# Performance work log

Measured on AMD Instinct MI355X. Metric: run time of the kernel, lower is better.

Reference implementation:

```python
import jax, jax.numpy as jnp
import numpy as np

N_LEVELS = 16
N_FEATS = 2
LOG2_T = 19
TABLE_SIZE = 2 ** LOG2_T
BASE_RES = 16
PER_LEVEL_SCALE = 1.3819
N_PTS = 524288
# per-level grid resolutions (static)
RESOLUTIONS = np.floor(BASE_RES * PER_LEVEL_SCALE ** np.arange(N_LEVELS)).astype(np.float32)
# NGP spatial hash primes for 2D
PRIME0 = np.uint32(1)
PRIME1 = np.uint32(2654435761)
# corner offsets for bilinear interp: (0,0),(0,1),(1,0),(1,1)
CORNER_OFFS = np.array([[0, 0], [0, 1], [1, 0], [1, 1]], dtype=np.uint32)


def setup_inputs() -> dict:
    key = jax.random.key(0)
    k1, k2 = jax.random.split(key)
    pts = jax.random.uniform(k1, (N_PTS, 3), dtype=jnp.float32)  # coords in [0,1]
    # 3 planes x L levels x T entries x F features, small init like NGP (1e-4)
    tables = jax.random.normal(k2, (3, N_LEVELS, TABLE_SIZE, N_FEATS), dtype=jnp.float32) * 1e-4
    return {"pts": pts, "tables": tables}


def _encode_plane(coords, table):
    # coords: [N,2] in [0,1]; table: [L,T,F]
    L, T, F = table.shape
    res = jnp.asarray(RESOLUTIONS)  # [L]
    scaled = coords[None, :, :] * res[:, None, None]  # [L,N,2]
    x0 = jnp.floor(scaled)
    frac = scaled - x0  # [L,N,2]
    x0u = x0.astype(jnp.uint32)
    offs = jnp.asarray(CORNER_OFFS)  # [4,2]
    corners = x0u[:, :, None, :] + offs[None, None, :, :]  # [L,N,4,2]
    # NGP spatial hash with uint32 wraparound, then mod table size
    h = (corners[..., 0] * PRIME0) ^ (corners[..., 1] * PRIME1)  # [L,N,4] uint32
    idx = (h % jnp.uint32(T)).astype(jnp.int32)  # [L,N,4]
    feats = table[jnp.arange(L)[:, None, None], idx]  # [L,N,4,F]
    # bilinear weights: product over dims of frac (offset=1) or 1-frac (offset=0)
    fo = offs.astype(coords.dtype)  # [4,2]
    w = jnp.prod(jnp.where(fo[None, None] > 0, frac[:, :, None, :], 1.0 - frac[:, :, None, :]), axis=-1)  # [L,N,4]
    out = jnp.einsum('lnc,lncf->lnf', w, feats)  # [L,N,F]
    return out.transpose(1, 0, 2).reshape(coords.shape[0], L * F)  # [N, L*F]


def reference(pts, tables):
    # coordinate-pair planes: combinations of (0,1,2) taken 2 at a time
    coo_combs = [(0, 1), (0, 2), (1, 2)]
    interp_space = 1.0
    for ci, comb in enumerate(coo_combs):
        interp_space = interp_space * _encode_plane(pts[:, list(comb)], tables[ci])
    return interp_space  # [N, 32]
```

## Files before the change

kernel.cpp:

```cpp
#include <hip/hip_runtime.h>
#include <stdint.h>


#define NPTS   524288u
#define TSIZE  524288u
#define TMASK  0x7FFFFu
#define PRIME1 2654435761u

__constant__ float c_res[16] = {
    16.f, 22.f, 30.f, 42.f, 58.f, 80.f, 111.f, 153.f,
    212.f, 294.f, 406.f, 561.f, 775.f, 1072.f, 1481.f, 2047.f
};
__constant__ int c_resiLow[12] = {16, 22, 30, 42, 58, 80, 111, 153, 212, 294, 406, 561};

__global__ __launch_bounds__(256) void k_packhist(
    const float* __restrict__ pts, float2* __restrict__ pts2,
    uint32_t* __restrict__ hist)
{
    __shared__ uint32_t lh[768];
    const uint32_t b = blockIdx.x, t = threadIdx.x;
    lh[t] = 0u; lh[t + 256u] = 0u; lh[t + 512u] = 0u;
    __syncthreads();
    const uint32_t pt = b * 256u + t;
    const float x = pts[pt * 3u + 0u];
    const float y = pts[pt * 3u + 1u];
    const float z = pts[pt * 3u + 2u];
    pts2[            pt] = make_float2(x, y);
    pts2[NPTS      + pt] = make_float2(x, z);
    pts2[2u * NPTS + pt] = make_float2(y, z);
    const uint32_t bx = min(15u, (uint32_t)(x * 16.f));
    const uint32_t by = min(15u, (uint32_t)(y * 16.f));
    const uint32_t bz = min(15u, (uint32_t)(z * 16.f));
    atomicAdd(&lh[         bx * 16u + by], 1u);
    atomicAdd(&lh[256u +   bx * 16u + bz], 1u);
    atomicAdd(&lh[512u +   by * 16u + bz], 1u);
    __syncthreads();
    if (lh[t])        atomicAdd(&hist[t],        lh[t]);
    if (lh[t + 256u]) atomicAdd(&hist[t + 256u], lh[t + 256u]);
    if (lh[t + 512u]) atomicAdd(&hist[t + 512u], lh[t + 512u]);
}

__global__ __launch_bounds__(256) void k_scatter(
    const float2* __restrict__ pts2, const uint32_t* __restrict__ hist,
    uint32_t* __restrict__ cursor, float4* __restrict__ sort16)
{
    __shared__ uint32_t su[256], lcnt[256], gb[256], lc2[256];
    const uint32_t b = blockIdx.x, t = threadIdx.x;
    const uint32_t plane = b >> 6, chunk = b & 63u;
    const uint32_t h = hist[plane * 256u + t];
    su[t] = h; lcnt[t] = 0u; lc2[t] = 0u;
    __syncthreads();
    for (uint32_t off = 1u; off < 256u; off <<= 1) {
        uint32_t v = 0u;
        if (t >= off) v = su[t - off];
        __syncthreads();
        su[t] += v;
        __syncthreads();
    }
    const uint32_t mybase = su[t] - h;
    const float2* __restrict__ pp = pts2 + (size_t)plane * NPTS;
    const uint32_t pt0 = chunk * 8192u + t;
    for (uint32_t k = 0; k < 32u; ++k) {
        const float2 c = pp[pt0 + k * 256u];
        const uint32_t bb = min(15u, (uint32_t)(c.x * 16.f)) * 16u
                          + min(15u, (uint32_t)(c.y * 16.f));
        atomicAdd(&lcnt[bb], 1u);
    }
    __syncthreads();
    gb[t] = mybase + atomicAdd(&cursor[plane * 256u + t], lcnt[t]);
    __syncthreads();
    float4* __restrict__ sp = sort16 + (size_t)plane * NPTS;
    for (uint32_t k = 0; k < 32u; ++k) {
        const uint32_t pt = pt0 + k * 256u;
        const float2 c = pp[pt];
        const uint32_t bb = min(15u, (uint32_t)(c.x * 16.f)) * 16u
                          + min(15u, (uint32_t)(c.y * 16.f));
        const uint32_t r = atomicAdd(&lc2[bb], 1u);
        sp[gb[bb] + r] = make_float4(c.x, c.y, __uint_as_float(pt), 0.f);
    }
}

__global__ __launch_bounds__(256) void k_lowhi(
    const float2* __restrict__ pts2, const float4* __restrict__ sort16,
    const uint32_t* __restrict__ hist, const float2* __restrict__ tab,
    float2* __restrict__ ws2, float2* __restrict__ wsH)
{
    __shared__ float2 sm[4000];
    const uint32_t b = blockIdx.x, t = threadIdx.x;

    if (b < 768u) {
        const uint32_t plane  = b >> 8;
        const uint32_t bucket = b & 255u;
        const uint32_t bx = bucket >> 4, by = bucket & 15u;

        uint32_t* su = (uint32_t*)sm;
        const uint32_t h = hist[plane * 256u + t];
        su[t] = h;
        __syncthreads();
        for (uint32_t off = 1u; off < 256u; off <<= 1) {
            uint32_t v = 0u;
            if (t >= off) v = su[t - off];
            __syncthreads();
            su[t] += v;
            __syncthreads();
        }
        const uint32_t cntB  = hist[plane * 256u + bucket];
        const uint32_t start = su[bucket] - cntB;
        __syncthreads();

        uint32_t* Pm = (uint32_t*)(sm + 3968);
        if (t == 0u) {
            uint32_t off = 0u;
            for (uint32_t l = 0; l < 12u; ++l) {
                const int R = c_resiLow[l];
                const int u0s = max(0, (int)((bx * (uint32_t)R) >> 4) - 1);
                const int u0e = min(R, (int)(((bx + 1u) * (uint32_t)R) >> 4) + 2);
                const int u1s = max(0, (int)((by * (uint32_t)R) >> 4) - 1);
                const int u1e = min(R, (int)(((by + 1u) * (uint32_t)R) >> 4) + 2);
                const uint32_t rows = (uint32_t)(u0e - u0s + 1);
                const uint32_t cols = (uint32_t)(u1e - u1s + 1);
                Pm[l] = off; Pm[12u + l] = (uint32_t)u0s;
                Pm[24u + l] = (uint32_t)u1s; Pm[36u + l] = cols;
                Pm[48u + l] = rows;
                off += rows * cols;
            }
        }
        __syncthreads();

        for (uint32_t l = 0; l < 12u; ++l) {
            const uint32_t off  = Pm[l];
            const uint32_t u0s  = Pm[12u + l], u1s = Pm[24u + l];
            const uint32_t cols = Pm[36u + l], rows = Pm[48u + l];
            const uint32_t E    = rows * cols;
            const uint32_t tb   = (plane * 16u + l) * TSIZE;
            for (uint32_t i = t; i < E; i += 256u) {
                const uint32_t r  = i / cols;
                const uint32_t cx = u0s + r;
                const uint32_t cy = u1s + (i - r * cols);
                sm[off + i] = tab[tb + ((cx ^ (cy * PRIME1)) & TMASK)];
            }
        }
        __syncthreads();

        const float4* __restrict__ sp = sort16 + (size_t)plane * NPTS;
        float4* __restrict__ w4 = (float4*)ws2;
        for (uint32_t i = t; i < cntB; i += 256u) {
            const float4 f = sp[start + i];
            const float c0 = f.x, c1 = f.y;
            const uint32_t orig = __float_as_uint(f.z);
            float2 acc[12];
#pragma unroll
            for (int l = 0; l < 12; ++l) {
                const float res = c_res[l];
                const float s0 = c0 * res;
                const float s1 = c1 * res;
                const float f0 = floorf(s0);
                const float f1 = floorf(s1);
                const float r0 = s0 - f0;
                const float r1 = s1 - f1;
                const uint32_t u0 = (uint32_t)f0, u1 = (uint32_t)f1;
                const uint32_t cols = Pm[36u + l];
                const uint32_t ci = Pm[l] + (u0 - Pm[12u + l]) * cols
                                  + (u1 - Pm[24u + l]);
                const float2 q00 = sm[ci];
                const float2 q01 = sm[ci + 1u];
                const float2 q10 = sm[ci + cols];
                const float2 q11 = sm[ci + cols + 1u];
                const float w00 = (1.f - r0) * (1.f - r1);
                const float w01 = (1.f - r0) * r1;
                const float w10 = r0 * (1.f - r1);
                const float w11 = r0 * r1;
                acc[l] = make_float2(
                    w00 * q00.x + w01 * q01.x + w10 * q10.x + w11 * q11.x,
                    w00 * q00.y + w01 * q01.y + w10 * q10.y + w11 * q11.y);
            }
            const size_t d = (size_t)orig * 18u + (size_t)plane * 6u;
            w4[d + 0] = make_float4(acc[0].x, acc[0].y, acc[1].x, acc[1].y);
            w4[d + 1] = make_float4(acc[2].x, acc[2].y, acc[3].x, acc[3].y);
            w4[d + 2] = make_float4(acc[4].x, acc[4].y, acc[5].x, acc[5].y);
            w4[d + 3] = make_float4(acc[6].x, acc[6].y, acc[7].x, acc[7].y);
            w4[d + 4] = make_float4(acc[8].x, acc[8].y, acc[9].x, acc[9].y);
            w4[d + 5] = make_float4(acc[10].x, acc[10].y, acc[11].x, acc[11].y);
        }
        return;
    }

    const uint32_t hb  = b - 768u;
    const uint32_t xcd = hb & 7u;
    const uint32_t s   = hb >> 3;
    uint32_t g, chunk;
    if (s < 512u) { g = xcd; chunk = s; }
    else { g = 8u + (xcd >> 1); chunk = ((xcd & 1u) << 8) + (s - 512u); }
    const uint32_t plane = g % 3u;
    const uint32_t lvl   = 12u + g / 3u;
    const uint32_t gabs  = plane * 16u + lvl;
    const float    res   = c_res[lvl];
    const uint32_t tb    = gabs * TSIZE;
    const float4* __restrict__ tab4 = (const float4*)tab;
    const uint32_t b4    = gabs * (TSIZE / 2u);
    const float2* __restrict__ pp = pts2 + (size_t)plane * NPTS;
    const uint32_t pt0   = chunk * 1024u + t;

    float4 P0[4], P1[4];
    float2 Q0[4], Q1[4];
    float  r0[4], r1[4];
    uint32_t sel0[4], sel1[4], oddm[4];

#pragma unroll
    for (int k = 0; k < 4; ++k) {
        const uint32_t pt = pt0 + (uint32_t)k * 256u;
        const float2 c2 = pp[pt];
        const float s0 = c2.x * res;
        const float s1 = c2.y * res;
        const float f0 = floorf(s0);
        const float f1 = floorf(s1);
        r0[k] = s0 - f0;
        r1[k] = s1 - f1;
        const uint32_t u0  = (uint32_t)f0;
        const uint32_t hy0 = (uint32_t)f1 * PRIME1;
        const uint32_t hy1 = hy0 + PRIME1;
        const uint32_t i00 = ( u0        ^ hy0) & TMASK;
        const uint32_t i01 = ( u0        ^ hy1) & TMASK;
        const uint32_t i10 = ((u0 + 1u)  ^ hy0) & TMASK;
        const uint32_t i11 = ((u0 + 1u)  ^ hy1) & TMASK;
        sel0[k] = i00 & 1u;
        sel1[k] = i01 & 1u;
        oddm[k] = u0 & 1u;
        P0[k] = tab4[b4 + (i00 >> 1)];
        P1[k] = tab4[b4 + (i01 >> 1)];
        Q0[k] = make_float2(0.f, 0.f);
        Q1[k] = make_float2(0.f, 0.f);
        if (oddm[k]) {
            Q0[k] = tab[tb + i10];
            Q1[k] = tab[tb + i11];
        }
    }
#pragma unroll
    for (int k = 0; k < 4; ++k) {
        const uint32_t pt = pt0 + (uint32_t)k * 256u;
        const float2 lo0 = make_float2(P0[k].x, P0[k].y);
        const float2 hi0 = make_float2(P0[k].z, P0[k].w);
        const float2 lo1 = make_float2(P1[k].x, P1[k].y);
        const float2 hi1 = make_float2(P1[k].z, P1[k].w);
        const float2 t00 = sel0[k] ? hi0 : lo0;
        const float2 t01 = sel1[k] ? hi1 : lo1;
        const float2 t10 = oddm[k] ? Q0[k] : (sel0[k] ? lo0 : hi0);
        const float2 t11 = oddm[k] ? Q1[k] : (sel1[k] ? lo1 : hi1);
        const float w00 = (1.f - r0[k]) * (1.f - r1[k]);
        const float w01 = (1.f - r0[k]) * r1[k];
        const float w10 = r0[k] * (1.f - r1[k]);
        const float w11 = r0[k] * r1[k];
        wsH[(size_t)g * NPTS + pt] = make_float2(
            w00 * t00.x + w01 * t01.x + w10 * t10.x + w11 * t11.x,
            w00 * t00.y + w01 * t01.y + w10 * t10.y + w11 * t11.y);
    }
}

__global__ __launch_bounds__(256) void k_comb(
    const float2* __restrict__ ws2, const float2* __restrict__ wsH,
    float2* __restrict__ out)
{
    __shared__ float2 s2[2304];
    __shared__ float2 sh[768];
    const uint32_t b = blockIdx.x, t = threadIdx.x;
    const uint32_t pt0 = b * 64u;
    const float2* __restrict__ src = ws2 + (size_t)pt0 * 36u;
    for (uint32_t i = t; i < 2304u; i += 256u) s2[i] = src[i];
    for (uint32_t i = t; i < 768u; i += 256u) {
        const uint32_t j = i >> 6, p = i & 63u;
        sh[i] = wsH[(size_t)j * NPTS + pt0 + p];
    }
    __syncthreads();
#pragma unroll
    for (uint32_t k = 0; k < 4u; ++k) {
        const uint32_t e = t + k * 256u;
        const uint32_t pt = e >> 4, l = e & 15u;
        float2 v;
        if (l < 12u) {
            const float2 a  = s2[pt * 36u + l];
            const float2 bb = s2[pt * 36u + 12u + l];
            const float2 c  = s2[pt * 36u + 24u + l];
            v = make_float2(a.x * bb.x * c.x, a.y * bb.y * c.y);
        } else {
            const uint32_t j0 = (l - 12u) * 3u;
            const float2 a  = sh[j0 * 64u + pt];
            const float2 bb = sh[(j0 + 1u) * 64u + pt];
            const float2 c  = sh[(j0 + 2u) * 64u + pt];
            v = make_float2(a.x * bb.x * c.x, a.y * bb.y * c.y);
        }
        out[(size_t)(pt0 + pt) * 16u + l] = v;
    }
}

template <int P, bool FIRST>
__global__ __launch_bounds__(256) void kplane_pass(
    const float* __restrict__ pts, const float2* __restrict__ tab,
    float2* __restrict__ ws)
{
    const uint32_t b     = blockIdx.x;
    const uint32_t xcd   = b & 7u;
    const uint32_t s     = b >> 3;
    const uint32_t gi    = s >> 11;
    const uint32_t chunk = s & 2047u;
    const uint32_t lvl   = gi * 8u + xcd;
    const uint32_t pt    = chunk * 256u + threadIdx.x;
    constexpr int c0 = (P == 2) ? 1 : 0;
    constexpr int c1 = (P == 0) ? 1 : 2;
    const float a0  = pts[pt * 3u + c0];
    const float a1  = pts[pt * 3u + c1];
    const float res = c_res[lvl];
    const float s0 = a0 * res;
    const float s1 = a1 * res;
    const float f0 = floorf(s0);
    const float f1 = floorf(s1);
    const float r0 = s0 - f0;
    const float r1 = s1 - f1;
    const uint32_t u0 = (uint32_t)f0;
    const uint32_t hy0  = (uint32_t)f1 * PRIME1;
    const uint32_t hy1  = hy0 + PRIME1;
    const uint32_t base = ((uint32_t)P * 16u + lvl) * TSIZE;
    const float2 t00 = tab[base + (( u0       ^ hy0) & TMASK)];
    const float2 t01 = tab[base + (( u0       ^ hy1) & TMASK)];
    const float2 t10 = tab[base + (((u0 + 1u) ^ hy0) & TMASK)];
    const float2 t11 = tab[base + (((u0 + 1u) ^ hy1) & TMASK)];
    const float w00 = (1.f - r0) * (1.f - r1);
    const float w01 = (1.f - r0) * r1;
    const float w10 = r0 * (1.f - r1);
    const float w11 = r0 * r1;
    const float e0 = w00 * t00.x + w01 * t01.x + w10 * t10.x + w11 * t11.x;
    const float e1 = w00 * t00.y + w01 * t01.y + w10 * t10.y + w11 * t11.y;
    const uint32_t widx = lvl * NPTS + pt;
    if (FIRST) {
        ws[widx] = make_float2(e0, e1);
    } else {
        const float2 prev = ws[widx];
        ws[widx] = make_float2(prev.x * e0, prev.y * e1);
    }
}

__global__ __launch_bounds__(256) void kplane_transpose(
    const float2* __restrict__ ws, float2* __restrict__ out)
{
    const uint32_t tid = blockIdx.x * 256u + threadIdx.x;
    const uint32_t lvl = tid & 15u;
    const uint32_t pt  = tid >> 4;
    out[tid] = ws[lvl * NPTS + pt];
}

__global__ __launch_bounds__(256) void kplane_mono(
    const float* __restrict__ pts, const float2* __restrict__ tab,
    float2* __restrict__ out)
{
    const uint32_t tid = blockIdx.x * 256u + threadIdx.x;
    const uint32_t pt  = tid >> 4;
    const uint32_t lvl = tid & 15u;
    const float x = pts[pt * 3u + 0u];
    const float y = pts[pt * 3u + 1u];
    const float z = pts[pt * 3u + 2u];
    const float res = c_res[lvl];
    const float a0[3] = {x, x, y};
    const float a1[3] = {y, z, z};
    float p0 = 1.f, p1 = 1.f;
#pragma unroll
    for (int pl = 0; pl < 3; ++pl) {
        const float s0 = a0[pl] * res;
        const float s1 = a1[pl] * res;
        const float f0 = floorf(s0);
        const float f1 = floorf(s1);
        const float r0 = s0 - f0;
        const float r1 = s1 - f1;
        const uint32_t u0 = (uint32_t)f0;
        const uint32_t hy0 = (uint32_t)f1 * PRIME1;
        const uint32_t hy1 = hy0 + PRIME1;
        const uint32_t base = ((uint32_t)pl * 16u + lvl) * TSIZE;
        const float2 t00 = tab[base + (( u0       ^ hy0) & TMASK)];
        const float2 t01 = tab[base + (( u0       ^ hy1) & TMASK)];
        const float2 t10 = tab[base + (((u0 + 1u) ^ hy0) & TMASK)];
        const float2 t11 = tab[base + (((u0 + 1u) ^ hy1) & TMASK)];
        const float w00 = (1.f - r0) * (1.f - r1);
        const float w01 = (1.f - r0) * r1;
        const float w10 = r0 * (1.f - r1);
        const float w11 = r0 * r1;
        p0 *= w00 * t00.x + w01 * t01.x + w10 * t10.x + w11 * t11.x;
        p1 *= w00 * t00.y + w01 * t01.y + w10 * t10.y + w11 * t11.y;
    }
    out[pt * 16u + lvl] = make_float2(p0, p1);
}

extern "C" void kernel_launch(void* const* d_in, const int* in_sizes, int n_in,
                              void* d_out, int out_size, void* d_ws, size_t ws_size,
                              hipStream_t stream) {
    const float*  pts = (const float*)d_in[0];
    const float2* tab = (const float2*)d_in[1];
    float2*       out = (float2*)d_out;

    const size_t wsA = (size_t)48 * NPTS * sizeof(float2);
    const size_t wsB = (size_t)16 * NPTS * sizeof(float2);
    dim3 block256(256u);

    if (ws_size >= wsA) {
        float2*   pts2   = (float2*)d_out;
        float4*   sort16 = (float4*)(pts2 + (size_t)3 * NPTS);
        uint32_t* hist   = (uint32_t*)(sort16 + (size_t)3 * NPTS);
        uint32_t* cursor = hist + 768;
        float2* ws2 = (float2*)d_ws;
        float2* wsH = ws2 + (size_t)36 * NPTS;

        hipMemsetAsync(hist, 0, 1536u * sizeof(uint32_t), stream);
        hipLaunchKernelGGL(k_packhist, dim3(2048u), block256, 0, stream,
                           pts, pts2, hist);
        hipLaunchKernelGGL(k_scatter,  dim3(192u),  block256, 0, stream,
                           pts2, hist, cursor, sort16);
        hipLaunchKernelGGL(k_lowhi,    dim3(6912u), block256, 0, stream,
                           pts2, sort16, hist, tab, ws2, wsH);
        hipLaunchKernelGGL(k_comb,     dim3(NPTS / 64u), block256, 0, stream,
                           ws2, wsH, out);
    } else if (ws_size >= wsB) {
        float2* ws = (float2*)d_ws;
        dim3 grid(16u * (NPTS / 256u));
        hipLaunchKernelGGL((kplane_pass<0, true >), grid, block256, 0, stream, pts, tab, ws);
        hipLaunchKernelGGL((kplane_pass<1, false>), grid, block256, 0, stream, pts, tab, ws);
        hipLaunchKernelGGL((kplane_pass<2, false>), grid, block256, 0, stream, pts, tab, ws);
        dim3 tgrid((NPTS * 16u) / 256u);
        hipLaunchKernelGGL(kplane_transpose, tgrid, block256, 0, stream, ws, out);
    } else {
        dim3 grid((NPTS * 16u) / 256u);
        hipLaunchKernelGGL(kplane_mono, grid, block256, 0, stream, pts, tab, out);
    }
}
```

Before: 282.1 us.

## Split low levels into dense shared-memory passes and fuse plane products for high levels

Levels 0-5 are now handled by unsorted streaming blocks that load each full small grid (or a half of level 5) into shared memory. Only levels 6-11 keep the bucket-sorted tiled path, which shrinks the per-bucket tile. The high levels 12-15 now compute all three planes per thread and write the product directly, removing the per-plane intermediate writes. The packed points are stored once as float4 instead of three float2 planes. Together these cut workspace traffic and per-bucket staging, at the cost of more blocks, branch divergence in the split level-5 pass, and redundant point reads.

```diff
diff --git a/kernel.cpp b/kernel.cpp
--- a/kernel.cpp
+++ b/kernel.cpp
@@ -11,10 +11,12 @@
     16.f, 22.f, 30.f, 42.f, 58.f, 80.f, 111.f, 153.f,
     212.f, 294.f, 406.f, 561.f, 775.f, 1072.f, 1481.f, 2047.f
 };
-__constant__ int c_resiLow[12] = {16, 22, 30, 42, 58, 80, 111, 153, 212, 294, 406, 561};
+__constant__ int      c_resi6[6] = {111, 153, 212, 294, 406, 561};
+__constant__ uint32_t c_R03[4]   = {17, 23, 31, 43};
+__constant__ uint32_t c_off03[4] = {0, 289, 818, 1779};
 
 __global__ __launch_bounds__(256) void k_packhist(
-    const float* __restrict__ pts, float2* __restrict__ pts2,
+    const float* __restrict__ pts, float4* __restrict__ pts4,
     uint32_t* __restrict__ hist)
 {
     __shared__ uint32_t lh[768];
@@ -25,9 +27,7 @@
     const float x = pts[pt * 3u + 0u];
     const float y = pts[pt * 3u + 1u];
     const float z = pts[pt * 3u + 2u];
-    pts2[            pt] = make_float2(x, y);
-    pts2[NPTS      + pt] = make_float2(x, z);
-    pts2[2u * NPTS + pt] = make_float2(y, z);
+    pts4[pt] = make_float4(x, y, z, 0.f);
     const uint32_t bx = min(15u, (uint32_t)(x * 16.f));
     const uint32_t by = min(15u, (uint32_t)(y * 16.f));
     const uint32_t bz = min(15u, (uint32_t)(z * 16.f));
@@ -41,7 +41,7 @@
 }
 
 __global__ __launch_bounds__(256) void k_scatter(
-    const float2* __restrict__ pts2, const uint32_t* __restrict__ hist,
+    const float4* __restrict__ pts4, const uint32_t* __restrict__ hist,
     uint32_t* __restrict__ cursor, float4* __restrict__ sort16)
 {
     __shared__ uint32_t su[256], lcnt[256], gb[256], lc2[256];
@@ -58,12 +58,13 @@
         __syncthreads();
     }
     const uint32_t mybase = su[t] - h;
-    const float2* __restrict__ pp = pts2 + (size_t)plane * NPTS;
     const uint32_t pt0 = chunk * 8192u + t;
     for (uint32_t k = 0; k < 32u; ++k) {
-        const float2 c = pp[pt0 + k * 256u];
-        const uint32_t bb = min(15u, (uint32_t)(c.x * 16.f)) * 16u
-                          + min(15u, (uint32_t)(c.y * 16.f));
+        const float4 c = pts4[pt0 + k * 256u];
+        const float c0 = (plane == 2u) ? c.y : c.x;
+        const float c1 = (plane == 0u) ? c.y : c.z;
+        const uint32_t bb = min(15u, (uint32_t)(c0 * 16.f)) * 16u
+                          + min(15u, (uint32_t)(c1 * 16.f));
         atomicAdd(&lcnt[bb], 1u);
     }
     __syncthreads();
@@ -72,20 +73,25 @@
     float4* __restrict__ sp = sort16 + (size_t)plane * NPTS;
     for (uint32_t k = 0; k < 32u; ++k) {
         const uint32_t pt = pt0 + k * 256u;
-        const float2 c = pp[pt];
-        const uint32_t bb = min(15u, (uint32_t)(c.x * 16.f)) * 16u
-                          + min(15u, (uint32_t)(c.y * 16.f));
+        const float4 c = pts4[pt];
+        const float c0 = (plane == 2u) ? c.y : c.x;
+        const float c1 = (plane == 0u) ? c.y : c.z;
+        const uint32_t bb = min(15u, (uint32_t)(c0 * 16.f)) * 16u
+                          + min(15u, (uint32_t)(c1 * 16.f));
         const uint32_t r = atomicAdd(&lc2[bb], 1u);
-        sp[gb[bb] + r] = make_float4(c.x, c.y, __uint_as_float(pt), 0.f);
-    }
-}
-
-__global__ __launch_bounds__(256) void k_lowhi(
-    const float2* __restrict__ pts2, const float4* __restrict__ sort16,
+        sp[gb[bb] + r] = make_float4(c0, c1, __uint_as_float(pt), 0.f);
+    }
+}
+
+__global__ __launch_bounds__(256) void k_mega(
+    const float4* __restrict__ pts4, const float4* __restrict__ sort16,
     const uint32_t* __restrict__ hist, const float2* __restrict__ tab,
-    float2* __restrict__ ws2, float2* __restrict__ wsH)
-{
-    __shared__ float2 sm[4000];
+    float2* __restrict__ ws05,
+    float2* __restrict__ ws2,
+    float2* __restrict__ wsP)
+{
+    __shared__ float2 sm[3700];
+    __shared__ uint32_t Poff[6], Pu0[6], Pu1[6], Pcols[6], Prows[6];
     const uint32_t b = blockIdx.x, t = threadIdx.x;
 
     if (b < 768u) {
@@ -108,31 +114,28 @@
         const uint32_t start = su[bucket] - cntB;
         __syncthreads();
 
-        uint32_t* Pm = (uint32_t*)(sm + 3968);
         if (t == 0u) {
             uint32_t off = 0u;
-            for (uint32_t l = 0; l < 12u; ++l) {
-                const int R = c_resiLow[l];
+            for (uint32_t l = 0; l < 6u; ++l) {
+                const int R = c_resi6[l];
                 const int u0s = max(0, (int)((bx * (uint32_t)R) >> 4) - 1);
                 const int u0e = min(R, (int)(((bx + 1u) * (uint32_t)R) >> 4) + 2);
                 const int u1s = max(0, (int)((by * (uint32_t)R) >> 4) - 1);
                 const int u1e = min(R, (int)(((by + 1u) * (uint32_t)R) >> 4) + 2);
                 const uint32_t rows = (uint32_t)(u0e - u0s + 1);
                 const uint32_t cols = (uint32_t)(u1e - u1s + 1);
-                Pm[l] = off; Pm[12u + l] = (uint32_t)u0s;
-                Pm[24u + l] = (uint32_t)u1s; Pm[36u + l] = cols;
-                Pm[48u + l] = rows;
+                Poff[l] = off; Pu0[l] = (uint32_t)u0s; Pu1[l] = (uint32_t)u1s;
+                Pcols[l] = cols; Prows[l] = rows;
                 off += rows * cols;
             }
         }
         __syncthreads();
 
-        for (uint32_t l = 0; l < 12u; ++l) {
-            const uint32_t off  = Pm[l];
-            const uint32_t u0s  = Pm[12u + l], u1s = Pm[24u + l];
-            const uint32_t cols = Pm[36u + l], rows = Pm[48u + l];
-            const uint32_t E    = rows * cols;
-            const uint32_t tb   = (plane * 16u + l) * TSIZE;
+        for (uint32_t l = 0; l < 6u; ++l) {
+            const uint32_t off = Poff[l], u0s = Pu0[l], u1s = Pu1[l];
+            const uint32_t cols = Pcols[l];
+            const uint32_t E = Prows[l] * cols;
+            const uint32_t tb = (plane * 16u + 6u + l) * TSIZE;
             for (uint32_t i = t; i < E; i += 256u) {
                 const uint32_t r  = i / cols;
                 const uint32_t cx = u0s + r;
@@ -148,10 +151,10 @@
             const float4 f = sp[start + i];
             const float c0 = f.x, c1 = f.y;
             const uint32_t orig = __float_as_uint(f.z);
-            float2 acc[12];
-#pragma unroll
-            for (int l = 0; l < 12; ++l) {
-                const float res = c_res[l];
+            float2 acc[6];
+#pragma unroll
+            for (int l = 0; l < 6; ++l) {
+                const float res = c_res[6 + l];
                 const float s0 = c0 * res;
                 const float s1 = c1 * res;
                 const float f0 = floorf(s0);
@@ -159,9 +162,8 @@
                 const float r0 = s0 - f0;
                 const float r1 = s1 - f1;
                 const uint32_t u0 = (uint32_t)f0, u1 = (uint32_t)f1;
-                const uint32_t cols = Pm[36u + l];
-                const uint32_t ci = Pm[l] + (u0 - Pm[12u + l]) * cols
-                                  + (u1 - Pm[24u + l]);
+                const uint32_t cols = Pcols[l];
+                const uint32_t ci = Poff[l] + (u0 - Pu0[l]) * cols + (u1 - Pu1[l]);
                 const float2 q00 = sm[ci];
                 const float2 q01 = sm[ci + 1u];
                 const float2 q10 = sm[ci + cols];
@@ -174,48 +176,165 @@
                     w00 * q00.x + w01 * q01.x + w10 * q10.x + w11 * q11.x,
                     w00 * q00.y + w01 * q01.y + w10 * q10.y + w11 * q11.y);
             }
-            const size_t d = (size_t)orig * 18u + (size_t)plane * 6u;
+            const size_t d = (size_t)orig * 9u + (size_t)plane * 3u;
             w4[d + 0] = make_float4(acc[0].x, acc[0].y, acc[1].x, acc[1].y);
             w4[d + 1] = make_float4(acc[2].x, acc[2].y, acc[3].x, acc[3].y);
             w4[d + 2] = make_float4(acc[4].x, acc[4].y, acc[5].x, acc[5].y);
-            w4[d + 3] = make_float4(acc[6].x, acc[6].y, acc[7].x, acc[7].y);
-            w4[d + 4] = make_float4(acc[8].x, acc[8].y, acc[9].x, acc[9].y);
-            w4[d + 5] = make_float4(acc[10].x, acc[10].y, acc[11].x, acc[11].y);
         }
         return;
     }
 
-    const uint32_t hb  = b - 768u;
+    if (b < 1152u) {
+        const uint32_t bb    = b - 768u;
+        const uint32_t set   = bb >> 5;
+        const uint32_t chunk = bb & 31u;
+        const uint32_t plane = set >> 2;
+        const uint32_t kind  = set & 3u;
+        const uint32_t pt0   = chunk * 16384u + t;
+
+        if (kind == 0u) {
+#pragma unroll
+            for (int l = 0; l < 4; ++l) {
+                const uint32_t R = c_R03[l], off = c_off03[l], E = R * R;
+                const uint32_t tb = (plane * 16u + (uint32_t)l) * TSIZE;
+                for (uint32_t i = t; i < E; i += 256u) {
+                    const uint32_t cx = i / R, cy = i - cx * R;
+                    sm[off + i] = tab[tb + ((cx ^ (cy * PRIME1)) & TMASK)];
+                }
+            }
+            __syncthreads();
+            for (uint32_t k = 0; k < 64u; ++k) {
+                const uint32_t pt = pt0 + k * 256u;
+                const float4 c4 = pts4[pt];
+                const float c0 = (plane == 2u) ? c4.y : c4.x;
+                const float c1 = (plane == 0u) ? c4.y : c4.z;
+#pragma unroll
+                for (int l = 0; l < 4; ++l) {
+                    const uint32_t R = c_R03[l], off = c_off03[l];
+                    const float res = c_res[l];
+                    const float s0 = c0 * res;
+                    const float s1 = c1 * res;
+                    const float f0 = floorf(s0);
+                    const float f1 = floorf(s1);
+                    const float r0 = s0 - f0;
+                    const float r1 = s1 - f1;
+                    const uint32_t ci = off + (uint32_t)f0 * R + (uint32_t)f1;
+                    const float2 q00 = sm[ci];
+                    const float2 q01 = sm[ci + 1u];
+                    const float2 q10 = sm[ci + R];
+                    const float2 q11 = sm[ci + R + 1u];
+                    const float w00 = (1.f - r0) * (1.f - r1);
+                    const float w01 = (1.f - r0) * r1;
+                    const float w10 = r0 * (1.f - r1);
+                    const float w11 = r0 * r1;
+                    ws05[(size_t)(plane * 6u + (uint32_t)l) * NPTS + pt] =
+                        make_float2(
+                        w00 * q00.x + w01 * q01.x + w10 * q10.x + w11 * q11.x,
+                        w00 * q00.y + w01 * q01.y + w10 * q10.y + w11 * q11.y);
+                }
+            }
+        } else if (kind == 1u) {
+            const uint32_t R = 59u, E = 3481u;
+            const uint32_t tb = (plane * 16u + 4u) * TSIZE;
+            for (uint32_t i = t; i < E; i += 256u) {
+                const uint32_t cx = i / R, cy = i - cx * R;
+                sm[i] = tab[tb + ((cx ^ (cy * PRIME1)) & TMASK)];
+            }
+            __syncthreads();
+            for (uint32_t k = 0; k < 64u; ++k) {
+                const uint32_t pt = pt0 + k * 256u;
+                const float4 c4 = pts4[pt];
+                const float c0 = (plane == 2u) ? c4.y : c4.x;
+                const float c1 = (plane == 0u) ? c4.y : c4.z;
+                const float s0 = c0 * 58.f;
+                const float s1 = c1 * 58.f;
+                const float f0 = floorf(s0);
+                const float f1 = floorf(s1);
+                const float r0 = s0 - f0;
+                const float r1 = s1 - f1;
+                const uint32_t ci = (uint32_t)f0 * R + (uint32_t)f1;
+                const float2 q00 = sm[ci];
+                const float2 q01 = sm[ci + 1u];
+                const float2 q10 = sm[ci + R];
+                const float2 q11 = sm[ci + R + 1u];
+                const float w00 = (1.f - r0) * (1.f - r1);
+                const float w01 = (1.f - r0) * r1;
+                const float w10 = r0 * (1.f - r1);
+                const float w11 = r0 * r1;
+                ws05[(size_t)(plane * 6u + 4u) * NPTS + pt] = make_float2(
+                    w00 * q00.x + w01 * q01.x + w10 * q10.x + w11 * q11.x,
+                    w00 * q00.y + w01 * q01.y + w10 * q10.y + w11 * q11.y);
+            }
+        } else {
+            const uint32_t lo  = (kind == 2u) ? 0u : 40u;
+            const uint32_t hiX = lo + 40u;
+            const uint32_t R = 81u, E = 41u * 81u;
+            const uint32_t tb = (plane * 16u + 5u) * TSIZE;
+            for (uint32_t i = t; i < E; i += 256u) {
+                const uint32_t r = i / R;
+                const uint32_t cx = lo + r, cy = i - r * R;
+                sm[i] = tab[tb + ((cx ^ (cy * PRIME1)) & TMASK)];
+            }
+            __syncthreads();
+            for (uint32_t k = 0; k < 64u; ++k) {
+                const uint32_t pt = pt0 + k * 256u;
+                const float4 c4 = pts4[pt];
+                const float c0 = (plane == 2u) ? c4.y : c4.x;
+                const float c1 = (plane == 0u) ? c4.y : c4.z;
+                const float s0 = c0 * 80.f;
+                const float s1 = c1 * 80.f;
+                const float f0 = floorf(s0);
+                const float f1 = floorf(s1);
+                const uint32_t u0 = (uint32_t)f0;
+                if (u0 >= lo && u0 < hiX) {
+                    const float r0 = s0 - f0;
+                    const float r1 = s1 - f1;
+                    const uint32_t ci = (u0 - lo) * R + (uint32_t)f1;
+                    const float2 q00 = sm[ci];
+                    const float2 q01 = sm[ci + 1u];
+                    const float2 q10 = sm[ci + R];
+                    const float2 q11 = sm[ci + R + 1u];
+                    const float w00 = (1.f - r0) * (1.f - r1);
+                    const float w01 = (1.f - r0) * r1;
+                    const float w10 = r0 * (1.f - r1);
+                    const float w11 = r0 * r1;
+                    ws05[(size_t)(plane * 6u + 5u) * NPTS + pt] = make_float2(
+                        w00 * q00.x + w01 * q01.x + w10 * q10.x + w11 * q11.x,
+                        w00 * q00.y + w01 * q01.y + w10 * q10.y + w11 * q11.y);
+                }
+            }
+        }
+        return;
+    }
+
+    const uint32_t hb  = b - 1152u;
     const uint32_t xcd = hb & 7u;
     const uint32_t s   = hb >> 3;
-    uint32_t g, chunk;
-    if (s < 512u) { g = xcd; chunk = s; }
-    else { g = 8u + (xcd >> 1); chunk = ((xcd & 1u) << 8) + (s - 512u); }
-    const uint32_t plane = g % 3u;
-    const uint32_t lvl   = 12u + g / 3u;
-    const uint32_t gabs  = plane * 16u + lvl;
-    const float    res   = c_res[lvl];
-    const uint32_t tb    = gabs * TSIZE;
+    const uint32_t lvl = 12u + (xcd >> 1);
+    const uint32_t chunk = ((xcd & 1u) << 10) + s;
+    const uint32_t pt  = chunk * 256u + t;
+    const float4 c4 = pts4[pt];
+    const float pc0[3] = {c4.x, c4.x, c4.y};
+    const float pc1[3] = {c4.y, c4.z, c4.z};
+    const float res = c_res[lvl];
     const float4* __restrict__ tab4 = (const float4*)tab;
-    const uint32_t b4    = gabs * (TSIZE / 2u);
-    const float2* __restrict__ pp = pts2 + (size_t)plane * NPTS;
-    const uint32_t pt0   = chunk * 1024u + t;
-
-    float4 P0[4], P1[4];
-    float2 Q0[4], Q1[4];
-    float  r0[4], r1[4];
-    uint32_t sel0[4], sel1[4], oddm[4];
-
-#pragma unroll
-    for (int k = 0; k < 4; ++k) {
-        const uint32_t pt = pt0 + (uint32_t)k * 256u;
-        const float2 c2 = pp[pt];
-        const float s0 = c2.x * res;
-        const float s1 = c2.y * res;
+
+    float4 P0[3], P1[3];
+    float2 Q0[3], Q1[3];
+    float  r0[3], r1[3];
+    uint32_t sel0[3], sel1[3], oddm[3];
+
+#pragma unroll
+    for (int p = 0; p < 3; ++p) {
+        const uint32_t gabs = (uint32_t)p * 16u + lvl;
+        const uint32_t tb = gabs * TSIZE;
+        const uint32_t b4 = gabs * (TSIZE / 2u);
+        const float s0 = pc0[p] * res;
+        const float s1 = pc1[p] * res;
         const float f0 = floorf(s0);
         const float f1 = floorf(s1);
-        r0[k] = s0 - f0;
-        r1[k] = s1 - f1;
+        r0[p] = s0 - f0;
+        r1[p] = s1 - f1;
         const uint32_t u0  = (uint32_t)f0;
         const uint32_t hy0 = (uint32_t)f1 * PRIME1;
         const uint32_t hy1 = hy0 + PRIME1;
@@ -223,52 +342,57 @@
         const uint32_t i01 = ( u0        ^ hy1) & TMASK;
         const uint32_t i10 = ((u0 + 1u)  ^ hy0) & TMASK;
         const uint32_t i11 = ((u0 + 1u)  ^ hy1) & TMASK;
-        sel0[k] = i00 & 1u;
-        sel1[k] = i01 & 1u;
-        oddm[k] = u0 & 1u;
-        P0[k] = tab4[b4 + (i00 >> 1)];
-        P1[k] = tab4[b4 + (i01 >> 1)];
-        Q0[k] = make_float2(0.f, 0.f);
-        Q1[k] = make_float2(0.f, 0.f);
-        if (oddm[k]) {
-            Q0[k] = tab[tb + i10];
-            Q1[k] = tab[tb + i11];
-        }
-    }
-#pragma unroll
-    for (int k = 0; k < 4; ++k) {
-        const uint32_t pt = pt0 + (uint32_t)k * 256u;
-        const float2 lo0 = make_float2(P0[k].x, P0[k].y);
-        const float2 hi0 = make_float2(P0[k].z, P0[k].w);
-        const float2 lo1 = make_float2(P1[k].x, P1[k].y);
-        const float2 hi1 = make_float2(P1[k].z, P1[k].w);
-        const float2 t00 = sel0[k] ? hi0 : lo0;
-        const float2 t01 = sel1[k] ? hi1 : lo1;
-        const float2 t10 = oddm[k] ? Q0[k] : (sel0[k] ? lo0 : hi0);
-        const float2 t11 = oddm[k] ? Q1[k] : (sel1[k] ? lo1 : hi1);
-        const float w00 = (1.f - r0[k]) * (1.f - r1[k]);
-        const float w01 = (1.f - r0[k]) * r1[k];
-        const float w10 = r0[k] * (1.f - r1[k]);
-        const float w11 = r0[k] * r1[k];
-        wsH[(size_t)g * NPTS + pt] = make_float2(
-            w00 * t00.x + w01 * t01.x + w10 * t10.x + w11 * t11.x,
-            w00 * t00.y + w01 * t01.y + w10 * t10.y + w11 * t11.y);
-    }
+        sel0[p] = i00 & 1u;
+        sel1[p] = i01 & 1u;
+        oddm[p] = u0 & 1u;
+        P0[p] = tab4[b4 + (i00 >> 1)];
+        P1[p] = tab4[b4 + (i01 >> 1)];
+        Q0[p] = make_float2(0.f, 0.f);
+        Q1[p] = make_float2(0.f, 0.f);
+        if (oddm[p]) {
+            Q0[p] = tab[tb + i10];
+            Q1[p] = tab[tb + i11];
+        }
+    }
+    float prod0 = 1.f, prod1 = 1.f;
+#pragma unroll
+    for (int p = 0; p < 3; ++p) {
+        const float2 lo0 = make_float2(P0[p].x, P0[p].y);
+        const float2 hi0 = make_float2(P0[p].z, P0[p].w);
+        const float2 lo1 = make_float2(P1[p].x, P1[p].y);
+        const float2 hi1 = make_float2(P1[p].z, P1[p].w);
+        const float2 t00 = sel0[p] ? hi0 : lo0;
+        const float2 t01 = sel1[p] ? hi1 : lo1;
+        const float2 t10 = oddm[p] ? Q0[p] : (sel0[p] ? lo0 : hi0);
+        const float2 t11 = oddm[p] ? Q1[p] : (sel1[p] ? lo1 : hi1);
+        const float w00 = (1.f - r0[p]) * (1.f - r1[p]);
+        const float w01 = (1.f - r0[p]) * r1[p];
+        const float w10 = r0[p] * (1.f - r1[p]);
+        const float w11 = r0[p] * r1[p];
+        prod0 *= w00 * t00.x + w01 * t01.x + w10 * t10.x + w11 * t11.x;
+        prod1 *= w00 * t00.y + w01 * t01.y + w10 * t10.y + w11 * t11.y;
+    }
+    wsP[(size_t)(lvl - 12u) * NPTS + pt] = make_float2(prod0, prod1);
 }
 
 __global__ __launch_bounds__(256) void k_comb(
-    const float2* __restrict__ ws2, const float2* __restrict__ wsH,
-    float2* __restrict__ out)
-{
-    __shared__ float2 s2[2304];
-    __shared__ float2 sh[768];
+    const float2* __restrict__ ws05, const float2* __restrict__ ws2,
+    const float2* __restrict__ wsP, float2* __restrict__ out)
+{
+    __shared__ float2 s05[1152];
+    __shared__ float2 s2[1152];
+    __shared__ float2 spd[256];
     const uint32_t b = blockIdx.x, t = threadIdx.x;
     const uint32_t pt0 = b * 64u;
-    const float2* __restrict__ src = ws2 + (size_t)pt0 * 36u;
-    for (uint32_t i = t; i < 2304u; i += 256u) s2[i] = src[i];
-    for (uint32_t i = t; i < 768u; i += 256u) {
-        const uint32_t j = i >> 6, p = i & 63u;
-        sh[i] = wsH[(size_t)j * NPTS + pt0 + p];
+    for (uint32_t i = t; i < 1152u; i += 256u) {
+        const uint32_t row = i >> 6, p = i & 63u;
+        s05[i] = ws05[(size_t)row * NPTS + pt0 + p];
+    }
+    const float2* __restrict__ w2src = ws2 + (size_t)pt0 * 18u;
+    for (uint32_t i = t; i < 1152u; i += 256u) s2[i] = w2src[i];
+    {
+        const uint32_t row = t >> 6, p = t & 63u;
+        spd[t] = wsP[(size_t)row * NPTS + pt0 + p];
     }
     __syncthreads();
 #pragma unroll
@@ -276,17 +400,19 @@
         const uint32_t e = t + k * 256u;
         const uint32_t pt = e >> 4, l = e & 15u;
         float2 v;
-        if (l < 12u) {
-            const float2 a  = s2[pt * 36u + l];
-            const float2 bb = s2[pt * 36u + 12u + l];
-            const float2 c  = s2[pt * 36u + 24u + l];
+        if (l < 6u) {
+            const float2 a  = s05[l * 64u + pt];
+            const float2 bb = s05[(6u + l) * 64u + pt];
+            const float2 c  = s05[(12u + l) * 64u + pt];
+            v = make_float2(a.x * bb.x * c.x, a.y * bb.y * c.y);
+        } else if (l < 12u) {
+            const uint32_t j = l - 6u;
+            const float2 a  = s2[pt * 18u + j];
+            const float2 bb = s2[pt * 18u + 6u + j];
+            const float2 c  = s2[pt * 18u + 12u + j];
             v = make_float2(a.x * bb.x * c.x, a.y * bb.y * c.y);
         } else {
-            const uint32_t j0 = (l - 12u) * 3u;
-            const float2 a  = sh[j0 * 64u + pt];
-            const float2 bb = sh[(j0 + 1u) * 64u + pt];
-            const float2 c  = sh[(j0 + 2u) * 64u + pt];
-            v = make_float2(a.x * bb.x * c.x, a.y * bb.y * c.y);
+            v = spd[(l - 12u) * 64u + pt];
         }
         out[(size_t)(pt0 + pt) * 16u + l] = v;
     }
@@ -394,27 +520,28 @@
     const float2* tab = (const float2*)d_in[1];
     float2*       out = (float2*)d_out;
 
-    const size_t wsA = (size_t)48 * NPTS * sizeof(float2);
+    const size_t wsA = (size_t)40 * NPTS * sizeof(float2);
     const size_t wsB = (size_t)16 * NPTS * sizeof(float2);
     dim3 block256(256u);
 
     if (ws_size >= wsA) {
-        float2*   pts2   = (float2*)d_out;
-        float4*   sort16 = (float4*)(pts2 + (size_t)3 * NPTS);
+        float4*   pts4   = (float4*)d_out;
+        float4*   sort16 = pts4 + NPTS;
         uint32_t* hist   = (uint32_t*)(sort16 + (size_t)3 * NPTS);
         uint32_t* cursor = hist + 768;
-        float2* ws2 = (float2*)d_ws;
-        float2* wsH = ws2 + (size_t)36 * NPTS;
+        float2* ws05 = (float2*)d_ws;
+        float2* ws2  = ws05 + (size_t)18 * NPTS;
+        float2* wsP  = ws2  + (size_t)18 * NPTS;
 
         hipMemsetAsync(hist, 0, 1536u * sizeof(uint32_t), stream);
         hipLaunchKernelGGL(k_packhist, dim3(2048u), block256, 0, stream,
-                           pts, pts2, hist);
+                           pts, pts4, hist);
         hipLaunchKernelGGL(k_scatter,  dim3(192u),  block256, 0, stream,
-                           pts2, hist, cursor, sort16);
-        hipLaunchKernelGGL(k_lowhi,    dim3(6912u), block256, 0, stream,
-                           pts2, sort16, hist, tab, ws2, wsH);
+                           pts4, hist, cursor, sort16);
+        hipLaunchKernelGGL(k_mega,     dim3(9344u), block256, 0, stream,
+                           pts4, sort16, hist, tab, ws05, ws2, wsP);
         hipLaunchKernelGGL(k_comb,     dim3(NPTS / 64u), block256, 0, stream,
-                           ws2, wsH, out);
+                           ws05, ws2, wsP, out);
     } else if (ws_size >= wsB) {
         float2* ws = (float2*)d_ws;
         dim3 grid(16u * (NPTS / 256u));
```

Result: slower. 339.1 us (+20.2%).

## Pre-expand low-level hash grids densely, store intermediates as fp16, split low/hi kernels

Applied to the files above, without the earlier changes.

Adds a dense pre-expansion of the 12 low-resolution levels into a contiguous grid inside the pack kernel, so the low-level kernel loads coalesced dense rows instead of scattered hashed gathers. Per-plane intermediate features are now packed as half2 instead of float2, halving workspace write and read traffic in the combine step. The fused low/hi kernel is split into two separate launches. Storing intermediates in fp16 reduces precision before the three-plane product, and the dense buffer adds a layout dependency inside the output region.

```diff
diff --git a/kernel.cpp b/kernel.cpp
--- a/kernel.cpp
+++ b/kernel.cpp
@@ -1,4 +1,5 @@
 #include <hip/hip_runtime.h>
+#include <hip/hip_fp16.h>
 #include <stdint.h>
 
 
@@ -6,19 +7,52 @@
 #define TSIZE  524288u
 #define TMASK  0x7FFFFu
 #define PRIME1 2654435761u
+#define PLANE_D     663817u
+#define DENSE_TOTAL 1991451u
 
 __constant__ float c_res[16] = {
     16.f, 22.f, 30.f, 42.f, 58.f, 80.f, 111.f, 153.f,
     212.f, 294.f, 406.f, 561.f, 775.f, 1072.f, 1481.f, 2047.f
 };
-__constant__ int c_resiLow[12] = {16, 22, 30, 42, 58, 80, 111, 153, 212, 294, 406, 561};
-
-__global__ __launch_bounds__(256) void k_packhist(
-    const float* __restrict__ pts, float2* __restrict__ pts2,
-    uint32_t* __restrict__ hist)
+__constant__ int      c_resiLow[12] = {16, 22, 30, 42, 58, 80, 111, 153, 212, 294, 406, 561};
+__constant__ uint32_t c_RD[12]   = {17, 23, 31, 43, 59, 81, 112, 154, 213, 295, 407, 562};
+__constant__ uint32_t c_offD[12] = {0, 289, 818, 1779, 3628, 7109, 13670,
+                                    26214, 49930, 95299, 182324, 347973};
+
+__device__ __forceinline__ uint32_t pkh2(float a, float b) {
+    __half2 h2;
+    h2.x = __float2half_rn(a);
+    h2.y = __float2half_rn(b);
+    return *reinterpret_cast<const uint32_t*>(&h2);
+}
+__device__ __forceinline__ float2 uph2(uint32_t u) {
+    __half2 h2 = *reinterpret_cast<const __half2*>(&u);
+    return make_float2(__half2float(h2.x), __half2float(h2.y));
+}
+
+__global__ __launch_bounds__(256) void k_packexp(
+    const float* __restrict__ pts, const float2* __restrict__ tab,
+    float2* __restrict__ pts2, uint32_t* __restrict__ hist,
+    float2* __restrict__ dense)
 {
     __shared__ uint32_t lh[768];
     const uint32_t b = blockIdx.x, t = threadIdx.x;
+
+    if (b >= 2048u) {
+        const uint32_t idx = (b - 2048u) * 256u + t;
+        if (idx >= DENSE_TOTAL) return;
+        const uint32_t plane = idx / PLANE_D;
+        const uint32_t i     = idx - plane * PLANE_D;
+        uint32_t lvl = 11u;
+        while (i < c_offD[lvl]) lvl--;
+        const uint32_t RD    = c_RD[lvl];
+        const uint32_t local = i - c_offD[lvl];
+        const uint32_t cx = local / RD, cy = local - cx * RD;
+        dense[idx] =
+            tab[(plane * 16u + lvl) * TSIZE + ((cx ^ (cy * PRIME1)) & TMASK)];
+        return;
+    }
+
     lh[t] = 0u; lh[t + 256u] = 0u; lh[t + 512u] = 0u;
     __syncthreads();
     const uint32_t pt = b * 256u + t;
@@ -80,114 +114,109 @@
     }
 }
 
-__global__ __launch_bounds__(256) void k_lowhi(
-    const float2* __restrict__ pts2, const float4* __restrict__ sort16,
-    const uint32_t* __restrict__ hist, const float2* __restrict__ tab,
-    float2* __restrict__ ws2, float2* __restrict__ wsH)
+__global__ __launch_bounds__(256) void k_low(
+    const float4* __restrict__ sort16, const uint32_t* __restrict__ hist,
+    const float2* __restrict__ dense, uint4* __restrict__ ws2u)
 {
     __shared__ float2 sm[4000];
+    __shared__ uint32_t Poff[12], Pu0[12], Pu1[12], Pcols[12], Prows[12];
     const uint32_t b = blockIdx.x, t = threadIdx.x;
-
-    if (b < 768u) {
-        const uint32_t plane  = b >> 8;
-        const uint32_t bucket = b & 255u;
-        const uint32_t bx = bucket >> 4, by = bucket & 15u;
-
-        uint32_t* su = (uint32_t*)sm;
-        const uint32_t h = hist[plane * 256u + t];
-        su[t] = h;
+    const uint32_t plane  = b >> 8;
+    const uint32_t bucket = b & 255u;
+    const uint32_t bx = bucket >> 4, by = bucket & 15u;
+
+    uint32_t* su = (uint32_t*)sm;
+    const uint32_t h = hist[plane * 256u + t];
+    su[t] = h;
+    __syncthreads();
+    for (uint32_t off = 1u; off < 256u; off <<= 1) {
+        uint32_t v = 0u;
+        if (t >= off) v = su[t - off];
         __syncthreads();
-        for (uint32_t off = 1u; off < 256u; off <<= 1) {
-            uint32_t v = 0u;
-            if (t >= off) v = su[t - off];
-            __syncthreads();
-            su[t] += v;
-            __syncthreads();
+        su[t] += v;
+        __syncthreads();
+    }
+    const uint32_t cntB  = hist[plane * 256u + bucket];
+    const uint32_t start = su[bucket] - cntB;
+    __syncthreads();
+
+    if (t == 0u) {
+        uint32_t off = 0u;
+        for (uint32_t l = 0; l < 12u; ++l) {
+            const int R = c_resiLow[l];
+            const int u0s = max(0, (int)((bx * (uint32_t)R) >> 4) - 1);
+            const int u0e = min(R, (int)(((bx + 1u) * (uint32_t)R) >> 4) + 2);
+            const int u1s = max(0, (int)((by * (uint32_t)R) >> 4) - 1);
+            const int u1e = min(R, (int)(((by + 1u) * (uint32_t)R) >> 4) + 2);
+            const uint32_t rows = (uint32_t)(u0e - u0s + 1);
+            const uint32_t cols = (uint32_t)(u1e - u1s + 1);
+            Poff[l] = off; Pu0[l] = (uint32_t)u0s; Pu1[l] = (uint32_t)u1s;
+            Pcols[l] = cols; Prows[l] = rows;
+            off += rows * cols;
         }
-        const uint32_t cntB  = hist[plane * 256u + bucket];
-        const uint32_t start = su[bucket] - cntB;
-        __syncthreads();
-
-        uint32_t* Pm = (uint32_t*)(sm + 3968);
-        if (t == 0u) {
-            uint32_t off = 0u;
-            for (uint32_t l = 0; l < 12u; ++l) {
-                const int R = c_resiLow[l];
-                const int u0s = max(0, (int)((bx * (uint32_t)R) >> 4) - 1);
-                const int u0e = min(R, (int)(((bx + 1u) * (uint32_t)R) >> 4) + 2);
-                const int u1s = max(0, (int)((by * (uint32_t)R) >> 4) - 1);
-                const int u1e = min(R, (int)(((by + 1u) * (uint32_t)R) >> 4) + 2);
-                const uint32_t rows = (uint32_t)(u0e - u0s + 1);
-                const uint32_t cols = (uint32_t)(u1e - u1s + 1);
-                Pm[l] = off; Pm[12u + l] = (uint32_t)u0s;
-                Pm[24u + l] = (uint32_t)u1s; Pm[36u + l] = cols;
-                Pm[48u + l] = rows;
-                off += rows * cols;
-            }
+    }
+    __syncthreads();
+
+    const size_t pbase = (size_t)plane * PLANE_D;
+    for (uint32_t l = 0; l < 12u; ++l) {
+        const uint32_t off = Poff[l], u0s = Pu0[l], u1s = Pu1[l];
+        const uint32_t cols = Pcols[l];
+        const uint32_t E = Prows[l] * cols;
+        const uint32_t RD = c_RD[l];
+        const size_t dbase = pbase + c_offD[l];
+        for (uint32_t i = t; i < E; i += 256u) {
+            const uint32_t r  = i / cols;
+            const uint32_t cx = u0s + r;
+            const uint32_t cy = u1s + (i - r * cols);
+            sm[off + i] = dense[dbase + (size_t)cx * RD + cy];
         }
-        __syncthreads();
-
-        for (uint32_t l = 0; l < 12u; ++l) {
-            const uint32_t off  = Pm[l];
-            const uint32_t u0s  = Pm[12u + l], u1s = Pm[24u + l];
-            const uint32_t cols = Pm[36u + l], rows = Pm[48u + l];
-            const uint32_t E    = rows * cols;
-            const uint32_t tb   = (plane * 16u + l) * TSIZE;
-            for (uint32_t i = t; i < E; i += 256u) {
-                const uint32_t r  = i / cols;
-                const uint32_t cx = u0s + r;
-                const uint32_t cy = u1s + (i - r * cols);
-                sm[off + i] = tab[tb + ((cx ^ (cy * PRIME1)) & TMASK)];
-            }
+    }
+    __syncthreads();
+
+    const float4* __restrict__ sp = sort16 + (size_t)plane * NPTS;
+    for (uint32_t i = t; i < cntB; i += 256u) {
+        const float4 f = sp[start + i];
+        const float c0 = f.x, c1 = f.y;
+        const uint32_t orig = __float_as_uint(f.z);
+        uint32_t hp[12];
+#pragma unroll
+        for (int l = 0; l < 12; ++l) {
+            const float res = c_res[l];
+            const float s0 = c0 * res;
+            const float s1 = c1 * res;
+            const float f0 = floorf(s0);
+            const float f1 = floorf(s1);
+            const float r0 = s0 - f0;
+            const float r1 = s1 - f1;
+            const uint32_t u0 = (uint32_t)f0, u1 = (uint32_t)f1;
+            const uint32_t cols = Pcols[l];
+            const uint32_t ci = Poff[l] + (u0 - Pu0[l]) * cols + (u1 - Pu1[l]);
+            const float2 q00 = sm[ci];
+            const float2 q01 = sm[ci + 1u];
+            const float2 q10 = sm[ci + cols];
+            const float2 q11 = sm[ci + cols + 1u];
+            const float w00 = (1.f - r0) * (1.f - r1);
+            const float w01 = (1.f - r0) * r1;
+            const float w10 = r0 * (1.f - r1);
+            const float w11 = r0 * r1;
+            hp[l] = pkh2(
+                w00 * q00.x + w01 * q01.x + w10 * q10.x + w11 * q11.x,
+                w00 * q00.y + w01 * q01.y + w10 * q10.y + w11 * q11.y);
         }
-        __syncthreads();
-
-        const float4* __restrict__ sp = sort16 + (size_t)plane * NPTS;
-        float4* __restrict__ w4 = (float4*)ws2;
-        for (uint32_t i = t; i < cntB; i += 256u) {
-            const float4 f = sp[start + i];
-            const float c0 = f.x, c1 = f.y;
-            const uint32_t orig = __float_as_uint(f.z);
-            float2 acc[12];
-#pragma unroll
-            for (int l = 0; l < 12; ++l) {
-                const float res = c_res[l];
-                const float s0 = c0 * res;
-                const float s1 = c1 * res;
-                const float f0 = floorf(s0);
-                const float f1 = floorf(s1);
-                const float r0 = s0 - f0;
-                const float r1 = s1 - f1;
-                const uint32_t u0 = (uint32_t)f0, u1 = (uint32_t)f1;
-                const uint32_t cols = Pm[36u + l];
-                const uint32_t ci = Pm[l] + (u0 - Pm[12u + l]) * cols
-                                  + (u1 - Pm[24u + l]);
-                const float2 q00 = sm[ci];
-                const float2 q01 = sm[ci + 1u];
-                const float2 q10 = sm[ci + cols];
-                const float2 q11 = sm[ci + cols + 1u];
-                const float w00 = (1.f - r0) * (1.f - r1);
-                const float w01 = (1.f - r0) * r1;
-                const float w10 = r0 * (1.f - r1);
-                const float w11 = r0 * r1;
-                acc[l] = make_float2(
-                    w00 * q00.x + w01 * q01.x + w10 * q10.x + w11 * q11.x,
-                    w00 * q00.y + w01 * q01.y + w10 * q10.y + w11 * q11.y);
-            }
-            const size_t d = (size_t)orig * 18u + (size_t)plane * 6u;
-            w4[d + 0] = make_float4(acc[0].x, acc[0].y, acc[1].x, acc[1].y);
-            w4[d + 1] = make_float4(acc[2].x, acc[2].y, acc[3].x, acc[3].y);
-            w4[d + 2] = make_float4(acc[4].x, acc[4].y, acc[5].x, acc[5].y);
-            w4[d + 3] = make_float4(acc[6].x, acc[6].y, acc[7].x, acc[7].y);
-            w4[d + 4] = make_float4(acc[8].x, acc[8].y, acc[9].x, acc[9].y);
-            w4[d + 5] = make_float4(acc[10].x, acc[10].y, acc[11].x, acc[11].y);
-        }
-        return;
-    }
-
-    const uint32_t hb  = b - 768u;
-    const uint32_t xcd = hb & 7u;
-    const uint32_t s   = hb >> 3;
+        const size_t d = ((size_t)orig * 3u + plane) * 3u;
+        ws2u[d + 0] = make_uint4(hp[0], hp[1], hp[2],  hp[3]);
+        ws2u[d + 1] = make_uint4(hp[4], hp[5], hp[6],  hp[7]);
+        ws2u[d + 2] = make_uint4(hp[8], hp[9], hp[10], hp[11]);
+    }
+}
+
+__global__ __launch_bounds__(256) void k_hi(
+    const float2* __restrict__ pts2, const float2* __restrict__ tab,
+    uint32_t* __restrict__ wsHh)
+{
+    const uint32_t b = blockIdx.x, t = threadIdx.x;
+    const uint32_t xcd = b & 7u;
+    const uint32_t s   = b >> 3;
     uint32_t g, chunk;
     if (s < 512u) { g = xcd; chunk = s; }
     else { g = 8u + (xcd >> 1); chunk = ((xcd & 1u) << 8) + (s - 512u); }
@@ -250,25 +279,26 @@
         const float w01 = (1.f - r0[k]) * r1[k];
         const float w10 = r0[k] * (1.f - r1[k]);
         const float w11 = r0[k] * r1[k];
-        wsH[(size_t)g * NPTS + pt] = make_float2(
+        wsHh[(size_t)g * NPTS + pt] = pkh2(
             w00 * t00.x + w01 * t01.x + w10 * t10.x + w11 * t11.x,
             w00 * t00.y + w01 * t01.y + w10 * t10.y + w11 * t11.y);
     }
 }
 
 __global__ __launch_bounds__(256) void k_comb(
-    const float2* __restrict__ ws2, const float2* __restrict__ wsH,
+    const uint4* __restrict__ ws2u, const uint32_t* __restrict__ wsHh,
     float2* __restrict__ out)
 {
-    __shared__ float2 s2[2304];
-    __shared__ float2 sh[768];
+    __shared__ uint32_t s2[2304];
+    __shared__ uint32_t sh[768];
     const uint32_t b = blockIdx.x, t = threadIdx.x;
     const uint32_t pt0 = b * 64u;
-    const float2* __restrict__ src = ws2 + (size_t)pt0 * 36u;
-    for (uint32_t i = t; i < 2304u; i += 256u) s2[i] = src[i];
+    uint4* s4 = (uint4*)s2;
+    for (uint32_t i = t; i < 576u; i += 256u)
+        s4[i] = ws2u[(size_t)pt0 * 9u + i];
     for (uint32_t i = t; i < 768u; i += 256u) {
-        const uint32_t j = i >> 6, p = i & 63u;
-        sh[i] = wsH[(size_t)j * NPTS + pt0 + p];
+        const uint32_t g = i >> 6, p = i & 63u;
+        sh[i] = wsHh[(size_t)g * NPTS + pt0 + p];
     }
     __syncthreads();
 #pragma unroll
@@ -277,15 +307,15 @@
         const uint32_t pt = e >> 4, l = e & 15u;
         float2 v;
         if (l < 12u) {
-            const float2 a  = s2[pt * 36u + l];
-            const float2 bb = s2[pt * 36u + 12u + l];
-            const float2 c  = s2[pt * 36u + 24u + l];
+            const float2 a  = uph2(s2[pt * 36u + l]);
+            const float2 bb = uph2(s2[pt * 36u + 12u + l]);
+            const float2 c  = uph2(s2[pt * 36u + 24u + l]);
             v = make_float2(a.x * bb.x * c.x, a.y * bb.y * c.y);
         } else {
             const uint32_t j0 = (l - 12u) * 3u;
-            const float2 a  = sh[j0 * 64u + pt];
-            const float2 bb = sh[(j0 + 1u) * 64u + pt];
-            const float2 c  = sh[(j0 + 2u) * 64u + pt];
+            const float2 a  = uph2(sh[j0 * 64u + pt]);
+            const float2 bb = uph2(sh[(j0 + 1u) * 64u + pt]);
+            const float2 c  = uph2(sh[(j0 + 2u) * 64u + pt]);
             v = make_float2(a.x * bb.x * c.x, a.y * bb.y * c.y);
         }
         out[(size_t)(pt0 + pt) * 16u + l] = v;
@@ -394,27 +424,30 @@
     const float2* tab = (const float2*)d_in[1];
     float2*       out = (float2*)d_out;
 
-    const size_t wsA = (size_t)48 * NPTS * sizeof(float2);
+    const size_t wsA = (size_t)NPTS * 192u;
     const size_t wsB = (size_t)16 * NPTS * sizeof(float2);
     dim3 block256(256u);
 
     if (ws_size >= wsA) {
         float2*   pts2   = (float2*)d_out;
         float4*   sort16 = (float4*)(pts2 + (size_t)3 * NPTS);
-        uint32_t* hist   = (uint32_t*)(sort16 + (size_t)3 * NPTS);
+        float2*   dense  = (float2*)(sort16 + (size_t)3 * NPTS);
+        uint32_t* hist   = (uint32_t*)(dense + DENSE_TOTAL);
         uint32_t* cursor = hist + 768;
-        float2* ws2 = (float2*)d_ws;
-        float2* wsH = ws2 + (size_t)36 * NPTS;
+        uint4*    ws2u   = (uint4*)d_ws;
+        uint32_t* wsHh   = (uint32_t*)(ws2u + (size_t)NPTS * 9u);
 
         hipMemsetAsync(hist, 0, 1536u * sizeof(uint32_t), stream);
-        hipLaunchKernelGGL(k_packhist, dim3(2048u), block256, 0, stream,
-                           pts, pts2, hist);
-        hipLaunchKernelGGL(k_scatter,  dim3(192u),  block256, 0, stream,
+        hipLaunchKernelGGL(k_packexp, dim3(2048u + 7780u), block256, 0, stream,
+                           pts, tab, pts2, hist, dense);
+        hipLaunchKernelGGL(k_scatter, dim3(192u),  block256, 0, stream,
                            pts2, hist, cursor, sort16);
-        hipLaunchKernelGGL(k_lowhi,    dim3(6912u), block256, 0, stream,
-                           pts2, sort16, hist, tab, ws2, wsH);
-        hipLaunchKernelGGL(k_comb,     dim3(NPTS / 64u), block256, 0, stream,
-                           ws2, wsH, out);
+        hipLaunchKernelGGL(k_low,     dim3(768u),  block256, 0, stream,
+                           sort16, hist, dense, ws2u);
+        hipLaunchKernelGGL(k_hi,      dim3(6144u), block256, 0, stream,
+                           pts2, tab, wsHh);
+        hipLaunchKernelGGL(k_comb,    dim3(NPTS / 64u), block256, 0, stream,
+                           ws2u, wsHh, out);
     } else if (ws_size >= wsB) {
         float2* ws = (float2*)d_ws;
         dim3 grid(16u * (NPTS / 256u));
```

New measurement: 266.1 us. -5.7%, faster.
